# Kernel tuning notes

Measured on AMD Instinct MI355X. Metric: run time of the kernel, lower is better.

## Reference

```python
import jax, jax.numpy as jnp
import numpy as np
from jax import lax

B, CIN, COUT, K, N = 128, 32, 64, 3, 56
TAU, BETA = 0.5, 4.0


def _build_templates(n, tau, beta):
    # dist[mu_i, mu_j, i, j] = |i-mu_i| + |j-mu_j|
    r = np.arange(n)
    dist = np.abs(r[:, None, None, None] - r[None, None, :, None]) + \
           np.abs(r[None, :, None, None] - r[None, None, None, :])
    tpos = tau * np.maximum(1.0 - beta * dist / n, -1.0)          # [n,n,n,n]
    tpos = tpos.reshape(n * n, n, n).astype(np.float32)
    tneg = np.full((1, n, n), -tau, dtype=np.float32)
    return np.concatenate([tpos, tneg], axis=0)                   # [n*n+1, n, n]


def setup_inputs() -> dict:
    key = jax.random.key(0)
    k1, k2, k3 = jax.random.split(key, 3)
    x = jax.random.normal(k1, (B, CIN, N, N), dtype=jnp.float32)
    W = jax.random.normal(k2, (COUT, CIN, K, K), dtype=jnp.float32) * 0.05
    b = jax.random.normal(k3, (COUT,), dtype=jnp.float32) * 0.05
    templates = jnp.asarray(_build_templates(N, TAU, BETA))
    return {"x": x, "W": W, "b": b, "templates": templates}


def reference(x, W, b, templates):
    # conv2d padding=1, stride 1 + ReLU
    y = lax.conv_general_dilated(
        x, W, window_strides=(1, 1), padding=[(1, 1), (1, 1)],
        dimension_numbers=("NCHW", "OIHW", "NCHW"))
    y = jax.nn.relu(y + b[None, :, None, None])                   # [B,C,H,W]
    Bc, C, H, Wd = y.shape
    # per-(batch,channel) argmax over flattened spatial map -> template index
    idx = jnp.argmax(y.reshape(Bc, C, H * Wd), axis=-1)           # [B,C] int
    masks = templates[idx]                                        # [B,C,H,W]
    masked = y * masks
    return masked * (masked > 0)
```

## Files before the change

### kernel.cpp

```cpp
#include <hip/hip_runtime.h>
#include <cstddef>

#define NSP   56
#define NPX   3136
#define CINN  32
#define COUTN 64
#define NB    128
#define CO_PB 8
#define ROWS  7
#define NSTRIP 8
#define THR   448
#define SROWS 9
#define XCOL  68

__global__ __launch_bounds__(256)
void wtrans(const float* __restrict__ W, float* __restrict__ w2)
{
    int idx = blockIdx.x * 256 + threadIdx.x;
    if (idx < COUTN * CINN * 9) {
        int co_l = idx & 7;
        int t    = idx >> 3;
        int c    = t & 31;
        t >>= 5;
        int kk   = t % 9;
        int cog  = t / 9;
        w2[idx] = W[(size_t)(cog * 8 + co_l) * (CINN * 9) + c * 9 + kk];
    }
}

__global__ __launch_bounds__(THR, 4)
void conv_emul_pass1(const float* __restrict__ x,
                     const float* __restrict__ w2,
                     const float* __restrict__ bias,
                     float* __restrict__ y,
                     int* __restrict__ amax)
{
    __shared__ float xs[SROWS][CINN][XCOL];
    __shared__ float rv[7][CO_PB];
    __shared__ int   ri[7][CO_PB];

    const int tid = threadIdx.x;
    const int ty  = tid >> 6;
    const int tx  = tid & 63;
    const int b       = blockIdx.x >> 3;
    const int cog     = blockIdx.x & 7;
    const int co_base = cog * CO_PB;

    const float* xb = x  + (size_t)b * CINN * NPX;
    const float* wq = w2 + (size_t)cog * (9 * CINN * CO_PB);

    const int sc = tid / 14;
    const int sv = tid - sc * 14;
    const float* xg = xb + (size_t)sc * NPX + 4 * sv;

    for (int t = tid; t < SROWS * CINN * 2; t += THR) {
        int rr  = t / (CINN * 2);
        int rem = t - rr * (CINN * 2);
        int c   = rem >> 1;
        xs[rr][c][(rem & 1) ? 60 : 3] = 0.f;
    }

    float v1[CO_PB]; int i1[CO_PB];
    #pragma unroll
    for (int co = 0; co < CO_PB; ++co) { v1[co] = -1.f; i1[co] = 0; }

    float* yo = y + (size_t)(b * COUTN + co_base) * NPX;

    #pragma unroll 1
    for (int g = 0; g < NSTRIP; ++g) {
        if (g) __syncthreads();

        #pragma unroll
        for (int rr = 0; rr < SROWS; ++rr) {
            int gr = 7 * g + rr - 1;
            float4 val = make_float4(0.f, 0.f, 0.f, 0.f);
            if ((unsigned)gr < (unsigned)NSP)
                val = *(const float4*)(xg + gr * NSP);
            *(float4*)&xs[rr][sc][4 + 4 * sv] = val;
        }
        __syncthreads();

        float acc[CO_PB];
        #pragma unroll
        for (int co = 0; co < CO_PB; ++co) acc[co] = 0.f;

        if (tx < NSP) {
            #pragma unroll
            for (int kh = 0; kh < 3; ++kh) {
                #pragma unroll
                for (int kw = 0; kw < 3; ++kw) {
                    float xv[CINN];
                    #pragma unroll
                    for (int c = 0; c < CINN; ++c)
                        xv[c] = xs[ty + kh][c][tx + kw + 3];
                    const float* wk = wq + (kh * 3 + kw) * (CINN * CO_PB);
                    #pragma unroll
                    for (int c = 0; c < CINN; ++c) {
                        #pragma unroll
                        for (int co = 0; co < CO_PB; ++co)
                            acc[co] = fmaf(xv[c], wk[c * CO_PB + co], acc[co]);
                    }
                }
            }
            int p = (7 * g + ty) * NSP + tx;
            #pragma unroll
            for (int co = 0; co < CO_PB; ++co) {
                float v = acc[co] + bias[co_base + co];
                v = fmaxf(v, 0.f);
                yo[(size_t)co * NPX + p] = v;
                if (v > v1[co]) { v1[co] = v; i1[co] = p; }
            }
        }
    }

    #pragma unroll
    for (int co = 0; co < CO_PB; ++co) {
        float bv = v1[co]; int bi = i1[co];
        #pragma unroll
        for (int off = 32; off > 0; off >>= 1) {
            float ov = __shfl_xor(bv, off);
            int   oi = __shfl_xor(bi, off);
            if (ov > bv || (ov == bv && oi < bi)) { bv = ov; bi = oi; }
        }
        if ((tid & 63) == 0) { rv[ty][co] = bv; ri[ty][co] = bi; }
    }
    __syncthreads();
    if (tid < CO_PB) {
        float bv = rv[0][tid]; int bi = ri[0][tid];
        #pragma unroll
        for (int w = 1; w < 7; ++w) {
            float ov = rv[w][tid]; int oi = ri[w][tid];
            if (ov > bv || (ov == bv && oi < bi)) { bv = ov; bi = oi; }
        }
        amax[b * COUTN + co_base + tid] = bi;
    }
}

__global__ __launch_bounds__(256)
void mask_apply_pass2(float* __restrict__ y,
                      const float* __restrict__ tmpl,
                      const int* __restrict__ amax)
{
    const int bc = blockIdx.x;
    const int idx = amax[bc];
    const float4* tp = (const float4*)(tmpl + (size_t)idx * NPX);
    float4* yp = (float4*)(y + (size_t)bc * NPX);
    #pragma unroll 1
    for (int p = threadIdx.x; p < NPX / 4; p += 256) {
        float4 a = yp[p];
        float4 t = tp[p];
        a.x *= t.x; a.y *= t.y; a.z *= t.z; a.w *= t.w;
        a.x = a.x > 0.f ? a.x : 0.f;
        a.y = a.y > 0.f ? a.y : 0.f;
        a.z = a.z > 0.f ? a.z : 0.f;
        a.w = a.w > 0.f ? a.w : 0.f;
        yp[p] = a;
    }
}

extern "C" void kernel_launch(void* const* d_in, const int* in_sizes, int n_in,
                              void* d_out, int out_size, void* d_ws, size_t ws_size,
                              hipStream_t stream)
{
    (void)in_sizes; (void)n_in; (void)ws_size; (void)out_size;
    const float* x  = (const float*)d_in[0];
    const float* W  = (const float*)d_in[1];
    const float* bi = (const float*)d_in[2];
    const float* tm = (const float*)d_in[3];
    float* out = (float*)d_out;
    int*   amax = (int*)d_ws;
    float* w2   = (float*)((char*)d_ws + 32768);

    hipLaunchKernelGGL(wtrans, dim3(72), dim3(256), 0, stream, W, w2);

    dim3 grid1(NB * (COUTN / CO_PB));
    hipLaunchKernelGGL(conv_emul_pass1, grid1, dim3(THR), 0, stream,
                       x, w2, bi, out, amax);

    dim3 grid2(NB * COUTN);
    hipLaunchKernelGGL(mask_apply_pass2, grid2, dim3(256), 0, stream,
                       out, tm, amax);
}
```

Measured before the change: 415.8 us.

## Use channel-interleaved swizzled LDS layout and two output rows per thread

Restructures the conv kernel so shared memory stores input as [row][col][channel] with an XOR swizzle, allowing float4 LDS reads of four channels at once. Each thread now computes two output rows (8-row strips, 256 threads), reusing each weight load across two accumulators, and bias is hoisted into registers. Global loads become strided scalar gathers across channels instead of coalesced float4 row loads, and register pressure doubles for accumulators with lower occupancy bounds.

```diff
diff --git a/kernel.cpp b/kernel.cpp
--- a/kernel.cpp
+++ b/kernel.cpp
@@ -7,11 +7,11 @@
 #define COUTN 64
 #define NB    128
 #define CO_PB 8
-#define ROWS  7
-#define NSTRIP 8
-#define THR   448
-#define SROWS 9
-#define XCOL  68
+#define ROWS  8
+#define NSTRIP 7
+#define THR   256
+#define SROWS 10
+#define SCOL  60
 
 __global__ __launch_bounds__(256)
 void wtrans(const float* __restrict__ W, float* __restrict__ w2)
@@ -28,19 +28,19 @@
     }
 }
 
-__global__ __launch_bounds__(THR, 4)
+__global__ __launch_bounds__(THR, 2)
 void conv_emul_pass1(const float* __restrict__ x,
                      const float* __restrict__ w2,
                      const float* __restrict__ bias,
                      float* __restrict__ y,
                      int* __restrict__ amax)
 {
-    __shared__ float xs[SROWS][CINN][XCOL];
-    __shared__ float rv[7][CO_PB];
-    __shared__ int   ri[7][CO_PB];
+    __shared__ float xs[SROWS * SCOL * 32];
+    __shared__ float rv[4][CO_PB];
+    __shared__ int   ri[4][CO_PB];
 
     const int tid = threadIdx.x;
-    const int ty  = tid >> 6;
+    const int wv  = tid >> 6;
     const int tx  = tid & 63;
     const int b       = blockIdx.x >> 3;
     const int cog     = blockIdx.x & 7;
@@ -49,16 +49,9 @@
     const float* xb = x  + (size_t)b * CINN * NPX;
     const float* wq = w2 + (size_t)cog * (9 * CINN * CO_PB);
 
-    const int sc = tid / 14;
-    const int sv = tid - sc * 14;
-    const float* xg = xb + (size_t)sc * NPX + 4 * sv;
-
-    for (int t = tid; t < SROWS * CINN * 2; t += THR) {
-        int rr  = t / (CINN * 2);
-        int rem = t - rr * (CINN * 2);
-        int c   = rem >> 1;
-        xs[rr][c][(rem & 1) ? 60 : 3] = 0.f;
-    }
+    float bs[CO_PB];
+    #pragma unroll
+    for (int co = 0; co < CO_PB; ++co) bs[co] = bias[co_base + co];
 
     float v1[CO_PB]; int i1[CO_PB];
     #pragma unroll
@@ -70,45 +63,76 @@
     for (int g = 0; g < NSTRIP; ++g) {
         if (g) __syncthreads();
 
+        #pragma unroll 1
+        for (int sr = 0; sr < SROWS; ++sr) {
+            int gr = 8 * g + sr - 1;
+            int gc = tx - 1;
+            bool vr = (unsigned)gr < (unsigned)NSP;
+            bool vc = (unsigned)gc < (unsigned)NSP;
+            #pragma unroll
+            for (int t = 0; t < 2; ++t) {
+                int qq = wv + 4 * t;
+                float4 v = make_float4(0.f, 0.f, 0.f, 0.f);
+                if (vr && vc) {
+                    const float* xp = xb + (size_t)(qq * 4) * NPX + gr * NSP + gc;
+                    v.x = xp[0];
+                    v.y = xp[NPX];
+                    v.z = xp[2 * NPX];
+                    v.w = xp[3 * NPX];
+                }
+                if (tx < SCOL) {
+                    int s = qq ^ (tx & 7);
+                    *(float4*)&xs[(sr * SCOL + tx) * 32 + s * 4] = v;
+                }
+            }
+        }
+        __syncthreads();
+
+        float acc0[CO_PB], acc1[CO_PB];
         #pragma unroll
-        for (int rr = 0; rr < SROWS; ++rr) {
-            int gr = 7 * g + rr - 1;
-            float4 val = make_float4(0.f, 0.f, 0.f, 0.f);
-            if ((unsigned)gr < (unsigned)NSP)
-                val = *(const float4*)(xg + gr * NSP);
-            *(float4*)&xs[rr][sc][4 + 4 * sv] = val;
-        }
-        __syncthreads();
-
-        float acc[CO_PB];
-        #pragma unroll
-        for (int co = 0; co < CO_PB; ++co) acc[co] = 0.f;
+        for (int co = 0; co < CO_PB; ++co) { acc0[co] = 0.f; acc1[co] = 0.f; }
 
         if (tx < NSP) {
             #pragma unroll
             for (int kh = 0; kh < 3; ++kh) {
                 #pragma unroll
                 for (int kw = 0; kw < 3; ++kw) {
-                    float xv[CINN];
-                    #pragma unroll
-                    for (int c = 0; c < CINN; ++c)
-                        xv[c] = xs[ty + kh][c][tx + kw + 3];
+                    const int col = tx + kw;
+                    const int cs  = col & 7;
+                    const int base0 = ((wv + kh)     * SCOL + col) * 32;
+                    const int base1 = ((wv + 4 + kh) * SCOL + col) * 32;
                     const float* wk = wq + (kh * 3 + kw) * (CINN * CO_PB);
                     #pragma unroll
-                    for (int c = 0; c < CINN; ++c) {
+                    for (int q = 0; q < 8; ++q) {
+                        int s = q ^ cs;
+                        float4 a4 = *(const float4*)&xs[base0 + s * 4];
+                        float4 b4 = *(const float4*)&xs[base1 + s * 4];
+                        const float av[4] = { a4.x, a4.y, a4.z, a4.w };
+                        const float bv[4] = { b4.x, b4.y, b4.z, b4.w };
                         #pragma unroll
-                        for (int co = 0; co < CO_PB; ++co)
-                            acc[co] = fmaf(xv[c], wk[c * CO_PB + co], acc[co]);
+                        for (int j = 0; j < 4; ++j) {
+                            const float* wc = wk + (q * 4 + j) * CO_PB;
+                            #pragma unroll
+                            for (int co = 0; co < CO_PB; ++co) {
+                                acc0[co] = fmaf(av[j], wc[co], acc0[co]);
+                                acc1[co] = fmaf(bv[j], wc[co], acc1[co]);
+                            }
+                        }
                     }
                 }
             }
-            int p = (7 * g + ty) * NSP + tx;
+            int p0 = (8 * g + wv) * NSP + tx;
+            int p1 = p0 + 4 * NSP;
             #pragma unroll
             for (int co = 0; co < CO_PB; ++co) {
-                float v = acc[co] + bias[co_base + co];
+                float v = acc0[co] + bs[co];
                 v = fmaxf(v, 0.f);
-                yo[(size_t)co * NPX + p] = v;
-                if (v > v1[co]) { v1[co] = v; i1[co] = p; }
+                yo[(size_t)co * NPX + p0] = v;
+                if (v > v1[co]) { v1[co] = v; i1[co] = p0; }
+                float u = acc1[co] + bs[co];
+                u = fmaxf(u, 0.f);
+                yo[(size_t)co * NPX + p1] = u;
+                if (u > v1[co]) { v1[co] = u; i1[co] = p1; }
             }
         }
     }
@@ -122,13 +146,13 @@
             int   oi = __shfl_xor(bi, off);
             if (ov > bv || (ov == bv && oi < bi)) { bv = ov; bi = oi; }
         }
-        if ((tid & 63) == 0) { rv[ty][co] = bv; ri[ty][co] = bi; }
+        if ((tid & 63) == 0) { rv[wv][co] = bv; ri[wv][co] = bi; }
     }
     __syncthreads();
     if (tid < CO_PB) {
         float bv = rv[0][tid]; int bi = ri[0][tid];
         #pragma unroll
-        for (int w = 1; w < 7; ++w) {
+        for (int w = 1; w < 4; ++w) {
             float ov = rv[w][tid]; int oi = ri[w][tid];
             if (ov > bv || (ov == bv && oi < bi)) { bv = ov; bi = oi; }
         }
```

After: 447.4 us. 1.08x slower.

## Widen output-channel tile and prefetch next strip into registers

Applied to the files above, without the earlier changes.

Each block now computes 16 output channels instead of 8, halving the number of blocks per batch. Each shared-memory load of the input window is reused across twice as many accumulators, and each input tile is staged half as often. The global loads for the next row strip are issued into registers before the current strip's compute and written to shared memory afterwards, so load latency overlaps with the FMAs. The shared tile row is also trimmed to 64 columns. The cost is much higher register pressure (16 accumulators plus argmax state plus the prefetch buffers), which risks spills or lower occupancy, and fewer blocks in the grid.

```diff
diff --git a/kernel.cpp b/kernel.cpp
--- a/kernel.cpp
+++ b/kernel.cpp
@@ -6,25 +6,25 @@
 #define CINN  32
 #define COUTN 64
 #define NB    128
-#define CO_PB 8
+#define CO_PB 16
 #define ROWS  7
 #define NSTRIP 8
 #define THR   448
 #define SROWS 9
-#define XCOL  68
+#define XCOL  64
 
 __global__ __launch_bounds__(256)
 void wtrans(const float* __restrict__ W, float* __restrict__ w2)
 {
     int idx = blockIdx.x * 256 + threadIdx.x;
     if (idx < COUTN * CINN * 9) {
-        int co_l = idx & 7;
-        int t    = idx >> 3;
+        int co_l = idx & 15;
+        int t    = idx >> 4;
         int c    = t & 31;
         t >>= 5;
         int kk   = t % 9;
         int cog  = t / 9;
-        w2[idx] = W[(size_t)(cog * 8 + co_l) * (CINN * 9) + c * 9 + kk];
+        w2[idx] = W[(size_t)(cog * CO_PB + co_l) * (CINN * 9) + c * 9 + kk];
     }
 }
 
@@ -42,8 +42,8 @@
     const int tid = threadIdx.x;
     const int ty  = tid >> 6;
     const int tx  = tid & 63;
-    const int b       = blockIdx.x >> 3;
-    const int cog     = blockIdx.x & 7;
+    const int b       = blockIdx.x >> 2;
+    const int cog     = blockIdx.x & 3;
     const int co_base = cog * CO_PB;
 
     const float* xb = x  + (size_t)b * CINN * NPX;
@@ -60,6 +60,21 @@
         xs[rr][c][(rem & 1) ? 60 : 3] = 0.f;
     }
 
+    {
+        float4 pf[SROWS];
+        #pragma unroll
+        for (int rr = 0; rr < SROWS; ++rr) {
+            int gr = rr - 1;
+            pf[rr] = make_float4(0.f, 0.f, 0.f, 0.f);
+            if ((unsigned)gr < (unsigned)NSP)
+                pf[rr] = *(const float4*)(xg + gr * NSP);
+        }
+        #pragma unroll
+        for (int rr = 0; rr < SROWS; ++rr)
+            *(float4*)&xs[rr][sc][4 + 4 * sv] = pf[rr];
+    }
+    __syncthreads();
+
     float v1[CO_PB]; int i1[CO_PB];
     #pragma unroll
     for (int co = 0; co < CO_PB; ++co) { v1[co] = -1.f; i1[co] = 0; }
@@ -68,17 +83,16 @@
 
     #pragma unroll 1
     for (int g = 0; g < NSTRIP; ++g) {
-        if (g) __syncthreads();
-
-        #pragma unroll
-        for (int rr = 0; rr < SROWS; ++rr) {
-            int gr = 7 * g + rr - 1;
-            float4 val = make_float4(0.f, 0.f, 0.f, 0.f);
-            if ((unsigned)gr < (unsigned)NSP)
-                val = *(const float4*)(xg + gr * NSP);
-            *(float4*)&xs[rr][sc][4 + 4 * sv] = val;
-        }
-        __syncthreads();
+        float4 nf[SROWS];
+        if (g < NSTRIP - 1) {
+            #pragma unroll
+            for (int rr = 0; rr < SROWS; ++rr) {
+                int gr = 7 * (g + 1) + rr - 1;
+                nf[rr] = make_float4(0.f, 0.f, 0.f, 0.f);
+                if ((unsigned)gr < (unsigned)NSP)
+                    nf[rr] = *(const float4*)(xg + gr * NSP);
+            }
+        }
 
         float acc[CO_PB];
         #pragma unroll
@@ -111,6 +125,14 @@
                 if (v > v1[co]) { v1[co] = v; i1[co] = p; }
             }
         }
+
+        __syncthreads();
+        if (g < NSTRIP - 1) {
+            #pragma unroll
+            for (int rr = 0; rr < SROWS; ++rr)
+                *(float4*)&xs[rr][sc][4 + 4 * sv] = nf[rr];
+            __syncthreads();
+        }
     }
 
     #pragma unroll
```

After: 469.5 us. +12.9%, slower.

## Replace LDS-staged conv tiles with direct per-pixel buffer loads

Applied to the files above, without the earlier changes.

Drops the shared-memory staging of input row strips and the barriers around it. Each thread now computes one flattened pixel per iteration and reads its 3x3x32 neighbourhood straight from global memory through raw buffer loads with range-checked descriptors, masking the padding in registers. Outputs are written through buffer stores, bias is hoisted into registers, and the occupancy hint is lowered from 4 to 2 blocks. This trades LDS traffic and synchronisation for many more global/L1 loads, roughly three per channel per kernel row, with heavy reuse that depends on the cache.

```diff
diff --git a/kernel.cpp b/kernel.cpp
--- a/kernel.cpp
+++ b/kernel.cpp
@@ -7,11 +7,26 @@
 #define COUTN 64
 #define NB    128
 #define CO_PB 8
-#define ROWS  7
-#define NSTRIP 8
 #define THR   448
-#define SROWS 9
-#define XCOL  68
+#define NIT   7
+
+typedef int v4i __attribute__((ext_vector_type(4)));
+
+__device__ float llvm_amdgcn_raw_buffer_load_f32(v4i rsrc, int voffset, int soffset, int aux)
+    __asm("llvm.amdgcn.raw.buffer.load.f32");
+__device__ void llvm_amdgcn_raw_buffer_store_f32(float data, v4i rsrc, int voffset, int soffset, int aux)
+    __asm("llvm.amdgcn.raw.buffer.store.f32");
+
+__device__ inline v4i make_rsrc(const void* p, int nbytes)
+{
+    union { const void* p; unsigned u[2]; } a; a.p = p;
+    v4i r;
+    r[0] = (int)a.u[0];
+    r[1] = (int)a.u[1];
+    r[2] = nbytes;
+    r[3] = 0x00020000;
+    return r;
+}
 
 __global__ __launch_bounds__(256)
 void wtrans(const float* __restrict__ W, float* __restrict__ w2)
@@ -28,88 +43,85 @@
     }
 }
 
-__global__ __launch_bounds__(THR, 4)
-void conv_emul_pass1(const float* __restrict__ x,
-                     const float* __restrict__ w2,
-                     const float* __restrict__ bias,
-                     float* __restrict__ y,
-                     int* __restrict__ amax)
+__global__ __launch_bounds__(THR, 2)
+void conv_px(const float* __restrict__ x,
+             const float* __restrict__ w2,
+             const float* __restrict__ bias,
+             float* __restrict__ y,
+             int* __restrict__ amax)
 {
-    __shared__ float xs[SROWS][CINN][XCOL];
-    __shared__ float rv[7][CO_PB];
-    __shared__ int   ri[7][CO_PB];
+    __shared__ float rvs[7][CO_PB];
+    __shared__ int   ris[7][CO_PB];
 
     const int tid = threadIdx.x;
     const int ty  = tid >> 6;
-    const int tx  = tid & 63;
     const int b       = blockIdx.x >> 3;
     const int cog     = blockIdx.x & 7;
     const int co_base = cog * CO_PB;
 
     const float* xb = x  + (size_t)b * CINN * NPX;
     const float* wq = w2 + (size_t)cog * (9 * CINN * CO_PB);
+    float* yo = y + (size_t)(b * COUTN + co_base) * NPX;
 
-    const int sc = tid / 14;
-    const int sv = tid - sc * 14;
-    const float* xg = xb + (size_t)sc * NPX + 4 * sv;
+    const v4i rx = make_rsrc(xb, CINN * NPX * 4);
+    const v4i ry = make_rsrc(yo, CO_PB * NPX * 4);
 
-    for (int t = tid; t < SROWS * CINN * 2; t += THR) {
-        int rr  = t / (CINN * 2);
-        int rem = t - rr * (CINN * 2);
-        int c   = rem >> 1;
-        xs[rr][c][(rem & 1) ? 60 : 3] = 0.f;
-    }
+    float bs[CO_PB];
+    #pragma unroll
+    for (int co = 0; co < CO_PB; ++co) bs[co] = bias[co_base + co];
 
     float v1[CO_PB]; int i1[CO_PB];
     #pragma unroll
     for (int co = 0; co < CO_PB; ++co) { v1[co] = -1.f; i1[co] = 0; }
 
-    float* yo = y + (size_t)(b * COUTN + co_base) * NPX;
-
     #pragma unroll 1
-    for (int g = 0; g < NSTRIP; ++g) {
-        if (g) __syncthreads();
-
-        #pragma unroll
-        for (int rr = 0; rr < SROWS; ++rr) {
-            int gr = 7 * g + rr - 1;
-            float4 val = make_float4(0.f, 0.f, 0.f, 0.f);
-            if ((unsigned)gr < (unsigned)NSP)
-                val = *(const float4*)(xg + gr * NSP);
-            *(float4*)&xs[rr][sc][4 + 4 * sv] = val;
-        }
-        __syncthreads();
+    for (int it = 0; it < NIT; ++it) {
+        const int p   = it * THR + tid;
+        const int row = p / NSP;
+        const int col = p - row * NSP;
+        const bool cL = (col > 0);
+        const bool cR = (col < NSP - 1);
 
         float acc[CO_PB];
         #pragma unroll
         for (int co = 0; co < CO_PB; ++co) acc[co] = 0.f;
 
-        if (tx < NSP) {
+        #pragma unroll
+        for (int kh = 0; kh < 3; ++kh) {
+            const int  r  = row + kh - 1;
+            const bool rv = ((unsigned)r < (unsigned)NSP);
+            const int  voff = (r * NSP + col) * 4;
+
+            float xm[CINN], xc[CINN], xp_[CINN];
             #pragma unroll
-            for (int kh = 0; kh < 3; ++kh) {
+            for (int c = 0; c < CINN; ++c) {
+                const int so = c * (NPX * 4);
+                float a = llvm_amdgcn_raw_buffer_load_f32(rx, voff - 4, so, 0);
+                float m = llvm_amdgcn_raw_buffer_load_f32(rx, voff,     so, 0);
+                float d = llvm_amdgcn_raw_buffer_load_f32(rx, voff + 4, so, 0);
+                xm[c]  = (rv && cL) ? a : 0.f;
+                xc[c]  =  rv        ? m : 0.f;
+                xp_[c] = (rv && cR) ? d : 0.f;
+            }
+            #pragma unroll
+            for (int kw = 0; kw < 3; ++kw) {
+                const float* wk = wq + (kh * 3 + kw) * (CINN * CO_PB);
                 #pragma unroll
-                for (int kw = 0; kw < 3; ++kw) {
-                    float xv[CINN];
+                for (int c = 0; c < CINN; ++c) {
+                    const float xv = (kw == 0) ? xm[c] : (kw == 1) ? xc[c] : xp_[c];
                     #pragma unroll
-                    for (int c = 0; c < CINN; ++c)
-                        xv[c] = xs[ty + kh][c][tx + kw + 3];
-                    const float* wk = wq + (kh * 3 + kw) * (CINN * CO_PB);
-                    #pragma unroll
-                    for (int c = 0; c < CINN; ++c) {
-                        #pragma unroll
-                        for (int co = 0; co < CO_PB; ++co)
-                            acc[co] = fmaf(xv[c], wk[c * CO_PB + co], acc[co]);
-                    }
+                    for (int co = 0; co < CO_PB; ++co)
+                        acc[co] = fmaf(xv, wk[c * CO_PB + co], acc[co]);
                 }
             }
-            int p = (7 * g + ty) * NSP + tx;
-            #pragma unroll
-            for (int co = 0; co < CO_PB; ++co) {
-                float v = acc[co] + bias[co_base + co];
-                v = fmaxf(v, 0.f);
-                yo[(size_t)co * NPX + p] = v;
-                if (v > v1[co]) { v1[co] = v; i1[co] = p; }
-            }
+        }
+
+        #pragma unroll
+        for (int co = 0; co < CO_PB; ++co) {
+            float v = acc[co] + bs[co];
+            v = fmaxf(v, 0.f);
+            llvm_amdgcn_raw_buffer_store_f32(v, ry, p * 4, co * (NPX * 4), 0);
+            if (v > v1[co]) { v1[co] = v; i1[co] = p; }
         }
     }
 
@@ -122,14 +134,14 @@
             int   oi = __shfl_xor(bi, off);
             if (ov > bv || (ov == bv && oi < bi)) { bv = ov; bi = oi; }
         }
-        if ((tid & 63) == 0) { rv[ty][co] = bv; ri[ty][co] = bi; }
+        if ((tid & 63) == 0) { rvs[ty][co] = bv; ris[ty][co] = bi; }
     }
     __syncthreads();
     if (tid < CO_PB) {
-        float bv = rv[0][tid]; int bi = ri[0][tid];
+        float bv = rvs[0][tid]; int bi = ris[0][tid];
         #pragma unroll
         for (int w = 1; w < 7; ++w) {
-            float ov = rv[w][tid]; int oi = ri[w][tid];
+            float ov = rvs[w][tid]; int oi = ris[w][tid];
             if (ov > bv || (ov == bv && oi < bi)) { bv = ov; bi = oi; }
         }
         amax[b * COUTN + co_base + tid] = bi;
@@ -174,7 +186,7 @@
     hipLaunchKernelGGL(wtrans, dim3(72), dim3(256), 0, stream, W, w2);
 
     dim3 grid1(NB * (COUTN / CO_PB));
-    hipLaunchKernelGGL(conv_emul_pass1, grid1, dim3(THR), 0, stream,
+    hipLaunchKernelGGL(conv_px, grid1, dim3(THR), 0, stream,
                        x, w2, bi, out, amax);
 
     dim3 grid2(NB * COUTN);
```

New measurement: 1.315 ms. +216.2%, slower.
